# Kernel optimization log

Measured on AMD Instinct MI355X. Metric: run time of the kernel, lower is better.

The kernel has to match this reference:

```python
import jax, jax.numpy as jnp
import numpy as np

H = 128; L = 4; B = 128; NPG = 32
N = B * NPG; E = B * NPG * NPG
NFREQ = 10; DIS = 2 * 3 * NFREQ; EIN = 2 * H + 9 + DIS  # 325


def setup_inputs() -> dict:
    key = jax.random.key(0)
    ks = jax.random.split(key, 16)
    atom_types = jax.random.randint(ks[0], (N,), 1, 101, dtype=jnp.int32)  # atomic numbers 1..100
    frac_coords = jax.random.uniform(ks[1], (N, 3), dtype=jnp.float32)
    lattices = jax.random.normal(ks[2], (B, 3, 3), dtype=jnp.float32)
    # fully-connected edges per graph incl. self-loops == block_diag(ones(n,n)) -> dense_to_sparse
    off = np.arange(B, dtype=np.int32)[:, None, None] * NPG
    rows = np.broadcast_to(np.arange(NPG, dtype=np.int32)[:, None], (NPG, NPG))
    cols = np.broadcast_to(np.arange(NPG, dtype=np.int32)[None, :], (NPG, NPG))
    edges = jnp.asarray(np.stack([(off + rows).reshape(E), (off + cols).reshape(E)]))
    node2graph = jnp.asarray(np.repeat(np.arange(B, dtype=np.int32), NPG))
    s = 0.02
    p = lambda k, shp: s * jax.random.normal(k, shp, dtype=jnp.float32)
    return dict(
        atom_types=atom_types, frac_coords=frac_coords, lattices=lattices,
        edges=edges, node2graph=node2graph,
        node_emb=p(ks[3], (100, H)),
        edge_w1=p(ks[4], (L, EIN, H)), edge_b1=jnp.zeros((L, H), jnp.float32),
        edge_w2=p(ks[5], (L, H, H)), edge_b2=jnp.zeros((L, H), jnp.float32),
        node_w1=p(ks[6], (L, 2 * H, H)), node_b1=jnp.zeros((L, H), jnp.float32),
        node_w2=p(ks[7], (L, H, H)), node_b2=jnp.zeros((L, H), jnp.float32),
        out_w=p(ks[8], (H, H)))


def _sin_emb(x):  # SinusoidsEmbedding: [E,3] -> [E, 2*3*NFREQ]
    freqs = 2.0 * jnp.pi * jnp.arange(NFREQ, dtype=x.dtype)
    e = (x[:, :, None] * freqs).reshape(x.shape[0], 3 * NFREQ)
    return jnp.concatenate([jnp.sin(e), jnp.cos(e)], axis=-1)


def reference(atom_types, frac_coords, lattices, edges, node2graph, node_emb,
              edge_w1, edge_b1, edge_w2, edge_b2,
              node_w1, node_b1, node_w2, node_b2, out_w):
    src, dst = edges[0], edges[1]
    frac_diff = frac_coords[dst] - frac_coords[src]            # gen_edges
    dis = jax.lax.stop_gradient(_sin_emb(frac_diff))           # dis_emb returns .detach()
    edge2graph = node2graph[src]
    lat_ip = jnp.einsum('bij,bkj->bik', lattices, lattices).reshape(-1, 9)  # ip=True
    lat_e = lat_ip[edge2graph]                                  # [E,9]
    h = node_emb[atom_types - 1]                                # [N,H]
    ones_e = jnp.ones((E,), h.dtype)
    cnt = jnp.clip(jax.ops.segment_sum(ones_e, src, num_segments=N), 1.0)[:, None]
    for l in range(L):  # CSPLayer, ln=False
        m = jnp.concatenate([h[src], h[dst], lat_e, dis], axis=-1)  # [E,325]
        m = jax.nn.silu(m @ edge_w1[l] + edge_b1[l])
        m = jax.nn.silu(m @ edge_w2[l] + edge_b2[l])                # edge features [E,H]
        agg = jax.ops.segment_sum(m, src, num_segments=N) / cnt     # scatter-mean onto edge_index[0]
        u = jnp.concatenate([h, agg], axis=-1)
        u = jax.nn.silu(u @ node_w1[l] + node_b1[l])
        u = jax.nn.silu(u @ node_w2[l] + node_b2[l])
        h = h + u                                                   # residual
    gcnt = jnp.clip(jax.ops.segment_sum(jnp.ones((N,), h.dtype), node2graph, num_segments=B), 1.0)[:, None]
    g = jax.ops.segment_sum(h, node2graph, num_segments=B) / gcnt   # scatter-mean pooling
    return g @ out_w                                                # out_node (no bias)
```

## Files before the change

### kernel.cpp

```cpp
#include <hip/hip_runtime.h>
#include <hip/hip_bf16.h>
#include <cstdint>

#define HH 128
#define LL 4
#define BB 128
#define NNODE 4096
#define EIN 325
#define NBLK 1024

#define OFF_W1  0
#define OFF_W2  80
#define OFF_NW1 112
#define OFF_NW2 176
#define FR_PER_L 208

typedef __attribute__((ext_vector_type(8))) short short8;
typedef __attribute__((ext_vector_type(4))) float float4v;

#define MFMA __builtin_amdgcn_mfma_f32_16x16x32_bf16

__device__ __forceinline__ uint32_t cvtpk2(float lo, float hi) {
    uint32_t r;
    asm("v_cvt_pk_bf16_f32 %0, %1, %2" : "=v"(r) : "v"(lo), "v"(hi));
    return r;
}
__device__ __forceinline__ uint16_t f2bf(float x) { return (uint16_t)cvtpk2(x, x); }

__device__ __forceinline__ float silu_f(float x) {
    float e;
    asm("v_exp_f32 %0, %1" : "=v"(e) : "v"(-1.44269504088896341f * x));
    float r;
    asm("v_rcp_f32 %0, %1" : "=v"(r) : "v"(1.0f + e));
    return x * r;
}

__device__ __forceinline__ short8 ldw(const uint4* wpl, int fidx, int lane) {
    return *reinterpret_cast<const short8*>(&wpl[(size_t)fidx*64 + lane]);
}

__global__ __launch_bounds__(256) void k_prep(
    const int* __restrict__ at, const float* __restrict__ frac,
    const float* __restrict__ lat, const float* __restrict__ emb,
    const float* __restrict__ ew1, const float* __restrict__ eb1,
    const float* __restrict__ ew2, const float* __restrict__ nw1,
    const float* __restrict__ nw2,
    uint4* __restrict__ disP, uint4* __restrict__ wp,
    float* __restrict__ h0, float* __restrict__ Cc)
{
    __shared__ uint16_t sm[8192];
    int gid = blockIdx.x, t = threadIdx.x;

    if (gid < 1024) {
        #pragma unroll
        for (int z = 0; z < 4; ++z) ((uint4*)sm)[t + 256*z] = uint4{0,0,0,0};
        __syncthreads();
        int b = gid >> 3, q4 = gid & 7;
        int e2 = t >> 1, half = t & 1;
        int i = q4*4 + (e2 >> 5), j = e2 & 31;
        float dx[3];
        #pragma unroll
        for (int d = 0; d < 3; ++d)
            dx[d] = frac[(b*32 + j)*3 + d] - frac[(b*32 + i)*3 + d];
        int T = e2 >> 4, rr = e2 & 15;
        #pragma unroll
        for (int kk = 0; kk < 30; ++kk) {
            int d = kk / 10, f = kk % 10;
            float ang = 6.28318530717958647692f * (float)f * dx[d];
            float v = half ? __cosf(ang) : __sinf(ang);
            int k = kk + 30*half;
            int ks = k >> 5, g = (k >> 3) & 3, ii = k & 7;
            sm[((ks*8 + T)*64 + g*16 + rr)*8 + ii] = f2bf(v);
        }
        __syncthreads();
        uint4* dst = disP + (size_t)gid * 1024;
        const uint4* smv = (const uint4*)sm;
        #pragma unroll
        for (int z = 0; z < 4; ++z) dst[t + 256*z] = smv[t + 256*z];
    } else if (gid < 1128) {
        int jidx = gid - 1024;
        int lay = jidx / 26, jj = jidx % 26;
        int wv = t >> 6, lane = t & 63, g = lane >> 4, col = lane & 15;
        int ks, base, type;
        if (jj < 10)      { ks = jj;      base = OFF_W1;  type = 0; }
        else if (jj < 14) { ks = jj - 10; base = OFF_W2;  type = 1; }
        else if (jj < 22) { ks = jj - 14; base = OFF_NW1; type = 2; }
        else              { ks = jj - 22; base = OFF_NW2; type = 3; }
        for (int nn = 0; nn < 2; ++nn) {
            int nf = 2*wv + nn;
            int n = nf*16 + col;
            uint16_t vals[8];
            #pragma unroll
            for (int ii = 0; ii < 8; ++ii) {
                int gk = 32*ks + 8*g + ii;
                float v = 0.f;
                if (type == 0) {
                    if (gk < 256)       v = ew1[((size_t)lay*EIN + gk)*HH + n];
                    else if (gk < 316)  v = ew1[((size_t)lay*EIN + gk + 9)*HH + n];
                } else if (type == 1)   v = ew2[((size_t)lay*HH + gk)*HH + n];
                else if (type == 2)     v = nw1[((size_t)lay*2*HH + gk)*HH + n];
                else                    v = nw2[((size_t)lay*HH + gk)*HH + n];
                vals[ii] = f2bf(v);
            }
            wp[((size_t)lay*FR_PER_L + base + ks*8 + nf)*64 + lane] = *(const uint4*)vals;
        }
    } else if (gid < 1640) {
        float* lip = (float*)sm;
        int blk = gid - 1128;
        int lay = blk >> 7, b = blk & 127;
        if (t < 9) {
            int i = t / 3, k2 = t % 3;
            const float* lb = lat + b*9;
            lip[t] = lb[i*3]*lb[k2*3] + lb[i*3+1]*lb[k2*3+1] + lb[i*3+2]*lb[k2*3+2];
        }
        __syncthreads();
        if (t < 128) {
            float acc = eb1[lay*HH + t];
            #pragma unroll
            for (int k = 0; k < 9; ++k)
                acc += lip[k] * ew1[((size_t)lay*EIN + 2*HH + k)*HH + t];
            Cc[(size_t)blk*HH + t] = acc;
        }
    } else {
        int idx = (gid - 1640)*256 + t;
        int n = idx >> 5, cq = idx & 31;
        float4v v = *(const float4v*)&emb[((size_t)(at[n]-1))*HH + cq*4];
        *(float4v*)&h0[(size_t)n*HH + cq*4] = v;
    }
}

__global__ __launch_bounds__(512, 4) void k_layer(
    const float* __restrict__ h_in, float* __restrict__ h_out,
    const uint4* __restrict__ disP, const uint4* __restrict__ wpl,
    const float* __restrict__ Cc_l, const float* __restrict__ b2,
    const float* __restrict__ nb1, const float* __restrict__ nb2)
{
    __shared__ uint4 smem4[2560];
    char* smem = (char*)smem4;
    char* hHi = smem;
    float* Af = (float*)(smem + 8192);
    float* Bf = (float*)(smem + 10304);
    char* sS  = smem + 8192;

    int bid = blockIdx.x;
    int b = bid >> 3, q4 = bid & 7;
    uint16_t* aggB = (uint16_t*)(smem + ((((q4 + 1) & 7)) << 10));
    uint16_t* u1B  = (uint16_t*)(smem + ((((q4 + 2) & 7)) << 10));
    int t = threadIdx.x;
    int w = t >> 6, l = t & 63;
    int wm = w >> 2, wn = w & 3;
    int g = l >> 4, rr = l & 15;

    short8 dfr[2][4];
    #pragma unroll
    for (int ks = 0; ks < 2; ++ks)
        #pragma unroll
        for (int mf = 0; mf < 4; ++mf)
            dfr[ks][mf] = *(const short8*)&disP[((size_t)(bid*2 + ks)*8 + 4*wm + mf)*64 + l];

    {
        int row = t >> 4, cz = (t & 15) * 8;
        const float* hp = h_in + (size_t)(b*32 + row)*HH + cz;
        float4v v0 = *(const float4v*)hp;
        float4v v1 = *(const float4v*)(hp + 4);
        uint32_t pw[4];
        pw[0] = cvtpk2(v0[0], v0[1]); pw[1] = cvtpk2(v0[2], v0[3]);
        pw[2] = cvtpk2(v1[0], v1[1]); pw[3] = cvtpk2(v1[2], v1[3]);
        *(uint4*)(hHi + row*256 + ((2*cz) ^ ((row & 7) << 4))) = *(const uint4*)pw;
    }
    __syncthreads();

    {
        float4v pacc[3];
        #pragma unroll
        for (int mt = 0; mt < 3; ++mt) pacc[mt] = (float4v){0.f,0.f,0.f,0.f};
        #pragma unroll
        for (int ks = 0; ks < 4; ++ks) {
            short8 wa = ldw(wpl, OFF_W1      + ks*8 + w, l);
            short8 wb = ldw(wpl, OFF_W1 + 32 + ks*8 + w, l);
            #pragma unroll
            for (int mt = 0; mt < 3; ++mt) {
                int R = (mt == 0) ? (q4*4 + (rr & 3)) : ((mt - 1)*16 + rr);
                short8 a = *(const short8*)(hHi + R*256 + ((64*ks + 16*g) ^ ((R & 7) << 4)));
                pacc[mt] = MFMA(a, (mt == 0) ? wa : wb, pacc[mt], 0, 0, 0);
            }
        }
        int n = 16*w + rr;
        if (g == 0) {
            #pragma unroll
            for (int r = 0; r < 4; ++r) Af[r*132 + n] = pacc[0][r];
        }
        #pragma unroll
        for (int r = 0; r < 4; ++r) Bf[(4*g + r)*132 + n]      = pacc[1][r];
        #pragma unroll
        for (int r = 0; r < 4; ++r) Bf[(16 + 4*g + r)*132 + n] = pacc[2][r];
    }
    __syncthreads();

    float ccv[2], b2v[2];
    #pragma unroll
    for (int nf = 0; nf < 2; ++nf) {
        ccv[nf] = Cc_l[b*HH + 32*wn + 16*nf + rr];
        b2v[nf] = b2[32*wn + 16*nf + rr];
    }

    float4v acc[4][2];
    #pragma unroll
    for (int mf = 0; mf < 4; ++mf) {
        int srcr = 2*wm + (mf >> 1);
        #pragma unroll
        for (int nf = 0; nf < 2; ++nf) {
            float iv = ccv[nf] + Af[srcr*132 + 32*wn + 16*nf + rr];
            acc[mf][nf] = (float4v){iv, iv, iv, iv};
        }
    }
    #pragma unroll
    for (int ks = 0; ks < 2; ++ks) {
        short8 wf[2];
        #pragma unroll
        for (int nf = 0; nf < 2; ++nf)
            wf[nf] = ldw(wpl, OFF_W1 + 64 + ks*8 + 2*wn + nf, l);
        #pragma unroll
        for (int mf = 0; mf < 4; ++mf)
            #pragma unroll
            for (int nf = 0; nf < 2; ++nf)
                acc[mf][nf] = MFMA(dfr[ks][mf], wf[nf], acc[mf][nf], 0, 0, 0);
    }
    #pragma unroll
    for (int mf = 0; mf < 4; ++mf)
        #pragma unroll
        for (int r = 0; r < 4; ++r) {
            const float* bp = &Bf[(16*(mf & 1) + 4*g + r)*132 + 32*wn + rr];
            #pragma unroll
            for (int nf = 0; nf < 2; ++nf)
                acc[mf][nf][r] += bp[16*nf];
        }
    __syncthreads();

    #pragma unroll
    for (int mf = 0; mf < 4; ++mf) {
        int T = 4*wm + mf;
        #pragma unroll
        for (int nf = 0; nf < 2; ++nf) {
            int n = 32*wn + 16*nf + rr;
            #pragma unroll
            for (int r = 0; r < 4; ++r) {
                int m = 16*T + 4*g + r;
                *(uint16_t*)(sS + m*256 + ((2*n) ^ ((m & 7) << 4))) = f2bf(silu_f(acc[mf][nf][r]));
            }
        }
    }
    __syncthreads();

    #pragma unroll
    for (int mf = 0; mf < 4; ++mf)
        #pragma unroll
        for (int nf = 0; nf < 2; ++nf)
            acc[mf][nf] = (float4v){0.f, 0.f, 0.f, 0.f};
    #pragma unroll
    for (int ks = 0; ks < 4; ++ks) {
        short8 wf[2];
        #pragma unroll
        for (int nf = 0; nf < 2; ++nf)
            wf[nf] = ldw(wpl, OFF_W2 + ks*8 + 2*wn + nf, l);
        #pragma unroll
        for (int mf = 0; mf < 4; ++mf) {
            int m = 16*(4*wm + mf) + rr;
            short8 a = *(const short8*)(sS + m*256 + ((64*ks + 16*g) ^ ((m & 7) << 4)));
            #pragma unroll
            for (int nf = 0; nf < 2; ++nf)
                acc[mf][nf] = MFMA(a, wf[nf], acc[mf][nf], 0, 0, 0);
        }
    }

    #pragma unroll
    for (int u = 0; u < 2; ++u) {
        #pragma unroll
        for (int nf = 0; nf < 2; ++nf) {
            float v = 0.f;
            #pragma unroll
            for (int mm = 0; mm < 2; ++mm)
                #pragma unroll
                for (int r = 0; r < 4; ++r)
                    v += silu_f(acc[2*u + mm][nf][r] + b2v[nf]);
            v += __shfl_xor(v, 16);
            v += __shfl_xor(v, 32);
            if (g == 0)
                aggB[(2*wm + u)*128 + 32*wn + 16*nf + rr] = f2bf(v * (1.0f/32.0f));
        }
    }
    __syncthreads();

    float4v uacc = (float4v){0.f, 0.f, 0.f, 0.f};
    #pragma unroll
    for (int ks = 0; ks < 8; ++ks) {
        short8 a;
        if (ks < 4) {
            int R = q4*4 + (rr & 3);
            a = *(const short8*)(hHi + R*256 + ((64*ks + 16*g) ^ ((R & 7) << 4)));
        } else {
            a = *(const short8*)&aggB[(rr & 3)*128 + 32*(ks - 4) + 8*g];
        }
        uacc = MFMA(a, ldw(wpl, OFF_NW1 + ks*8 + w, l), uacc, 0, 0, 0);
    }
    if (g == 0) {
        #pragma unroll
        for (int r = 0; r < 4; ++r) {
            int col = 16*w + rr;
            u1B[r*128 + col] = f2bf(silu_f(uacc[r] + nb1[col]));
        }
    }
    __syncthreads();

    float4v vacc = (float4v){0.f, 0.f, 0.f, 0.f};
    #pragma unroll
    for (int ks = 0; ks < 4; ++ks) {
        short8 a = *(const short8*)&u1B[(rr & 3)*128 + 32*ks + 8*g];
        vacc = MFMA(a, ldw(wpl, OFF_NW2 + ks*8 + w, l), vacc, 0, 0, 0);
    }
    if (g == 0) {
        #pragma unroll
        for (int r = 0; r < 4; ++r) {
            int col = 16*w + rr;
            size_t node = (size_t)(b*32 + q4*4 + r);
            h_out[node*HH + col] = h_in[node*HH + col] + silu_f(vacc[r] + nb2[col]);
        }
    }
}

__global__ __launch_bounds__(128) void k_pool(const float* __restrict__ h, const float* __restrict__ ow,
                       float* __restrict__ out) {
    __shared__ float sm_g[HH];
    int b = blockIdx.x, c = threadIdx.x;
    float s = 0.f;
    for (int n = 0; n < 32; ++n) s += h[(size_t)(b*32 + n)*HH + c];
    sm_g[c] = s * (1.0f/32.0f);
    __syncthreads();
    float acc = 0.f;
    for (int k = 0; k < HH; ++k) acc += sm_g[k] * ow[k*HH + c];
    out[(size_t)b*HH + c] = acc;
}

extern "C" void kernel_launch(void* const* d_in, const int* in_sizes, int n_in,
                              void* d_out, int out_size, void* d_ws, size_t ws_size,
                              hipStream_t stream) {
    const int*   atom_types = (const int*)d_in[0];
    const float* frac       = (const float*)d_in[1];
    const float* lat        = (const float*)d_in[2];
    const float* node_emb   = (const float*)d_in[5];
    const float* ew1        = (const float*)d_in[6];
    const float* eb1        = (const float*)d_in[7];
    const float* ew2        = (const float*)d_in[8];
    const float* eb2        = (const float*)d_in[9];
    const float* nw1        = (const float*)d_in[10];
    const float* nb1        = (const float*)d_in[11];
    const float* nw2        = (const float*)d_in[12];
    const float* nb2        = (const float*)d_in[13];
    const float* ow         = (const float*)d_in[14];
    float* out = (float*)d_out;

    char* ws = (char*)d_ws;
    uint4* disP = (uint4*)ws; ws += (size_t)NBLK*1024*16;
    uint4* wp   = (uint4*)ws; ws += (size_t)LL*FR_PER_L*64*16;
    float* hA   = (float*)ws; ws += (size_t)NNODE*HH*4;
    float* hB   = (float*)ws; ws += (size_t)NNODE*HH*4;
    float* Cc   = (float*)ws; ws += (size_t)LL*BB*HH*4;

    k_prep<<<2152, 256, 0, stream>>>(atom_types, frac, lat, node_emb,
                                     ew1, eb1, ew2, nw1, nw2,
                                     disP, wp, hA, Cc);

    float* hin = hA; float* hout = hB;
    for (int l = 0; l < LL; ++l) {
        k_layer<<<NBLK, 512, 0, stream>>>(hin, hout, disP, wp + (size_t)l*FR_PER_L*64,
                                          Cc + (size_t)l*BB*HH, eb2 + (size_t)l*HH,
                                          nb1 + (size_t)l*HH, nb2 + (size_t)l*HH);
        float* tmp = hin; hin = hout; hout = tmp;
    }
    k_pool<<<BB, HH, 0, stream>>>(hin, ow, out);
}
```

Before: 192.3 us.

## Fold per-node edge projections into edge GEMM and prefetch weights earlier

The first edge linear layer no longer computes the src/dst node projections once per node into shared memory and broadcasts them. It now issues the h[src]·W1a and h[dst]·W1b MFMAs directly into each edge tile's accumulator, which removes a barrier and the LDS staging, at the cost of roughly double the MFMA work for that stage. Weight fragments for the later GEMMs are loaded into registers ahead of the barriers so global-load latency can overlap with compute. Launch bounds are raised to request 8 waves-per-EU occupancy, which tightens the register budget.

```diff
diff --git a/kernel.cpp b/kernel.cpp
--- a/kernel.cpp
+++ b/kernel.cpp
@@ -129,7 +129,7 @@
     }
 }
 
-__global__ __launch_bounds__(512, 4) void k_layer(
+__global__ __launch_bounds__(512, 8) void k_layer(
     const float* __restrict__ h_in, float* __restrict__ h_out,
     const uint4* __restrict__ disP, const uint4* __restrict__ wpl,
     const float* __restrict__ Cc_l, const float* __restrict__ b2,
@@ -138,8 +138,6 @@
     __shared__ uint4 smem4[2560];
     char* smem = (char*)smem4;
     char* hHi = smem;
-    float* Af = (float*)(smem + 8192);
-    float* Bf = (float*)(smem + 10304);
     char* sS  = smem + 8192;
 
     int bid = blockIdx.x;
@@ -170,33 +168,6 @@
     }
     __syncthreads();
 
-    {
-        float4v pacc[3];
-        #pragma unroll
-        for (int mt = 0; mt < 3; ++mt) pacc[mt] = (float4v){0.f,0.f,0.f,0.f};
-        #pragma unroll
-        for (int ks = 0; ks < 4; ++ks) {
-            short8 wa = ldw(wpl, OFF_W1      + ks*8 + w, l);
-            short8 wb = ldw(wpl, OFF_W1 + 32 + ks*8 + w, l);
-            #pragma unroll
-            for (int mt = 0; mt < 3; ++mt) {
-                int R = (mt == 0) ? (q4*4 + (rr & 3)) : ((mt - 1)*16 + rr);
-                short8 a = *(const short8*)(hHi + R*256 + ((64*ks + 16*g) ^ ((R & 7) << 4)));
-                pacc[mt] = MFMA(a, (mt == 0) ? wa : wb, pacc[mt], 0, 0, 0);
-            }
-        }
-        int n = 16*w + rr;
-        if (g == 0) {
-            #pragma unroll
-            for (int r = 0; r < 4; ++r) Af[r*132 + n] = pacc[0][r];
-        }
-        #pragma unroll
-        for (int r = 0; r < 4; ++r) Bf[(4*g + r)*132 + n]      = pacc[1][r];
-        #pragma unroll
-        for (int r = 0; r < 4; ++r) Bf[(16 + 4*g + r)*132 + n] = pacc[2][r];
-    }
-    __syncthreads();
-
     float ccv[2], b2v[2];
     #pragma unroll
     for (int nf = 0; nf < 2; ++nf) {
@@ -206,14 +177,11 @@
 
     float4v acc[4][2];
     #pragma unroll
-    for (int mf = 0; mf < 4; ++mf) {
-        int srcr = 2*wm + (mf >> 1);
-        #pragma unroll
-        for (int nf = 0; nf < 2; ++nf) {
-            float iv = ccv[nf] + Af[srcr*132 + 32*wn + 16*nf + rr];
-            acc[mf][nf] = (float4v){iv, iv, iv, iv};
-        }
-    }
+    for (int mf = 0; mf < 4; ++mf)
+        #pragma unroll
+        for (int nf = 0; nf < 2; ++nf)
+            acc[mf][nf] = (float4v){ccv[nf], ccv[nf], ccv[nf], ccv[nf]};
+
     #pragma unroll
     for (int ks = 0; ks < 2; ++ks) {
         short8 wf[2];
@@ -227,14 +195,40 @@
                 acc[mf][nf] = MFMA(dfr[ks][mf], wf[nf], acc[mf][nf], 0, 0, 0);
     }
     #pragma unroll
-    for (int mf = 0; mf < 4; ++mf)
-        #pragma unroll
-        for (int r = 0; r < 4; ++r) {
-            const float* bp = &Bf[(16*(mf & 1) + 4*g + r)*132 + 32*wn + rr];
-            #pragma unroll
-            for (int nf = 0; nf < 2; ++nf)
-                acc[mf][nf][r] += bp[16*nf];
-        }
+    for (int ks = 0; ks < 4; ++ks) {
+        short8 wa[2], wb[2];
+        #pragma unroll
+        for (int nf = 0; nf < 2; ++nf) {
+            wa[nf] = ldw(wpl, OFF_W1      + ks*8 + 2*wn + nf, l);
+            wb[nf] = ldw(wpl, OFF_W1 + 32 + ks*8 + 2*wn + nf, l);
+        }
+        int offs = 64*ks + 16*g;
+        short8 sh[2], dh[2];
+        #pragma unroll
+        for (int p = 0; p < 2; ++p) {
+            int Rs = q4*4 + 2*wm + p;
+            sh[p] = *(const short8*)(hHi + Rs*256 + (offs ^ ((Rs & 7) << 4)));
+            int Rd = 16*p + rr;
+            dh[p] = *(const short8*)(hHi + Rd*256 + (offs ^ ((Rd & 7) << 4)));
+        }
+        #pragma unroll
+        for (int mf = 0; mf < 4; ++mf) {
+            int ps = mf >> 1, pd = mf & 1;
+            #pragma unroll
+            for (int nf = 0; nf < 2; ++nf) {
+                acc[mf][nf] = MFMA(sh[ps], wa[nf], acc[mf][nf], 0, 0, 0);
+                acc[mf][nf] = MFMA(dh[pd], wb[nf], acc[mf][nf], 0, 0, 0);
+            }
+        }
+    }
+
+    short8 wf2[4][2];
+    #pragma unroll
+    for (int ks = 0; ks < 4; ++ks)
+        #pragma unroll
+        for (int nf = 0; nf < 2; ++nf)
+            wf2[ks][nf] = ldw(wpl, OFF_W2 + ks*8 + 2*wn + nf, l);
+
     __syncthreads();
 
     #pragma unroll
@@ -259,19 +253,20 @@
             acc[mf][nf] = (float4v){0.f, 0.f, 0.f, 0.f};
     #pragma unroll
     for (int ks = 0; ks < 4; ++ks) {
-        short8 wf[2];
-        #pragma unroll
-        for (int nf = 0; nf < 2; ++nf)
-            wf[nf] = ldw(wpl, OFF_W2 + ks*8 + 2*wn + nf, l);
         #pragma unroll
         for (int mf = 0; mf < 4; ++mf) {
             int m = 16*(4*wm + mf) + rr;
             short8 a = *(const short8*)(sS + m*256 + ((64*ks + 16*g) ^ ((m & 7) << 4)));
             #pragma unroll
             for (int nf = 0; nf < 2; ++nf)
-                acc[mf][nf] = MFMA(a, wf[nf], acc[mf][nf], 0, 0, 0);
-        }
-    }
+                acc[mf][nf] = MFMA(a, wf2[ks][nf], acc[mf][nf], 0, 0, 0);
+        }
+    }
+
+    short8 wn1[8];
+    #pragma unroll
+    for (int ks = 0; ks < 8; ++ks)
+        wn1[ks] = ldw(wpl, OFF_NW1 + ks*8 + w, l);
 
     #pragma unroll
     for (int u = 0; u < 2; ++u) {
@@ -301,8 +296,13 @@
         } else {
             a = *(const short8*)&aggB[(rr & 3)*128 + 32*(ks - 4) + 8*g];
         }
-        uacc = MFMA(a, ldw(wpl, OFF_NW1 + ks*8 + w, l), uacc, 0, 0, 0);
-    }
+        uacc = MFMA(a, wn1[ks], uacc, 0, 0, 0);
+    }
+    short8 wn2[4];
+    #pragma unroll
+    for (int ks = 0; ks < 4; ++ks)
+        wn2[ks] = ldw(wpl, OFF_NW2 + ks*8 + w, l);
+
     if (g == 0) {
         #pragma unroll
         for (int r = 0; r < 4; ++r) {
@@ -316,7 +316,7 @@
     #pragma unroll
     for (int ks = 0; ks < 4; ++ks) {
         short8 a = *(const short8*)&u1B[(rr & 3)*128 + 32*ks + 8*g];
-        vacc = MFMA(a, ldw(wpl, OFF_NW2 + ks*8 + w, l), vacc, 0, 0, 0);
+        vacc = MFMA(a, wn2[ks], vacc, 0, 0, 0);
     }
     if (g == 0) {
         #pragma unroll
```

New measurement: 436.4 us. 2.27x slower.
